# Performance work log

Measured on AMD Instinct MI355X. Metric: run time of the kernel, lower is better.

The kernel has to match this reference:

```python
import jax, jax.numpy as jnp
import numpy as np

V_DIM = 2048
Q_DIM = 1024
B = 64
K = 36


def setup_inputs() -> dict:
    key = jax.random.key(0)
    ks = jax.random.split(key, 6)
    s1 = 1.0 / np.sqrt(2 * V_DIM + Q_DIM)
    s2 = 1.0 / np.sqrt(V_DIM)
    s3 = 1.0 / np.sqrt(Q_DIM)
    return {
        "v": jax.random.normal(ks[0], (B, K, V_DIM), dtype=jnp.float32),
        "q": jax.random.normal(ks[1], (B, Q_DIM), dtype=jnp.float32),
        "W1": jax.random.normal(ks[2], (V_DIM, 2 * V_DIM + Q_DIM), dtype=jnp.float32) * s1,
        "b1": jnp.zeros((V_DIM,), dtype=jnp.float32),
        "W2": jax.random.normal(ks[3], (V_DIM, V_DIM), dtype=jnp.float32) * s2,
        "b2": jnp.zeros((V_DIM,), dtype=jnp.float32),
        "W3": jax.random.normal(ks[4], (Q_DIM, Q_DIM), dtype=jnp.float32) * s3,
        "b3": jnp.zeros((Q_DIM,), dtype=jnp.float32),
    }


def reference(v, q, W1, b1, W2, b2, W3, b3):
    # FCNet = (weight-normed) Linear + ReLU; dropout disabled (eval / p=0).
    vd = W2.shape[0]
    # q embedding: [B, q_dim]
    q_emb = jax.nn.relu(q @ W3.T + b3)
    # Decompose linear1(concat(v_i, v_j, q_emb)) into three matmuls.
    Wa = W1[:, :vd]            # acts on v_i
    Wb = W1[:, vd:2 * vd]      # acts on v_j
    Wc = W1[:, 2 * vd:]        # acts on q_emb
    a = jnp.einsum('bkd,vd->bkv', v, Wa)          # [B, K, v_dim]
    bpart = jnp.einsum('bkd,vd->bkv', v, Wb)      # [B, K, v_dim]
    c = jnp.einsum('bq,vq->bv', q_emb, Wc) + b1   # [B, v_dim]
    # Pairwise ReLU then sum over j: [B, K_i, K_j, v_dim] -> [B, K, v_dim]
    pair = jax.nn.relu(a[:, :, None, :] + bpart[:, None, :, :] + c[:, None, None, :])
    x = jnp.sum(pair, axis=2)
    # linear2 + ReLU
    return jax.nn.relu(jnp.einsum('bkv,wv->bkw', x, W2) + b2)
```

## Files before the change

kernel.cpp:

```cpp
#include <hip/hip_runtime.h>

#define V_DIMC 2048
#define Q_DIMC 1024
#define BATCH  64
#define KC     36
#define MROWS  (BATCH * KC)
#define W1LD   (2 * V_DIMC + Q_DIMC)

typedef __bf16 bf16_t;
typedef __attribute__((ext_vector_type(8))) __bf16 bf16x8;
typedef __attribute__((ext_vector_type(4))) __bf16 bf16x4;
typedef __attribute__((ext_vector_type(4))) float f32x4;

__device__ __forceinline__ void gload16(const bf16_t* g, bf16_t* l) {
    __builtin_amdgcn_global_load_lds(
        (const __attribute__((address_space(1))) unsigned int*)(g),
        (__attribute__((address_space(3))) unsigned int*)(l), 16, 0, 0);
}

#define MFMAI(a, b, c) __builtin_amdgcn_mfma_f32_16x16x32_bf16(a, b, c, 0, 0, 0)
#define BARX() __builtin_amdgcn_s_barrier()
#define LGKM0() asm volatile("s_waitcnt lgkmcnt(0)" ::: "memory")
#define VMC(n)  asm volatile("s_waitcnt vmcnt(" #n ")" ::: "memory")

__global__ __launch_bounds__(256) void conv_all(const float* __restrict__ v,
                                                const float* __restrict__ q,
                                                const float* __restrict__ W1,
                                                const float* __restrict__ W2,
                                                const float* __restrict__ W3,
                                                bf16_t* __restrict__ Wab,
                                                bf16_t* __restrict__ W2b,
                                                bf16_t* __restrict__ vb,
                                                bf16_t* __restrict__ W3b,
                                                bf16_t* __restrict__ Wcb,
                                                bf16_t* __restrict__ qb) {
    const int t = blockIdx.x * 256 + threadIdx.x;
    const float* src;
    bf16_t* dst;
    if (t < 2097152) {
        size_t idx = (size_t)t * 4;
        int row = (int)(idx >> 11), col = (int)(idx & 2047);
        src = (row < 2048) ? W1 + (size_t)row * W1LD + col
                           : W1 + (size_t)(row - 2048) * W1LD + V_DIMC + col;
        dst = Wab + idx;
    } else if (t < 3145728) {
        size_t idx = (size_t)(t - 2097152) * 4;
        src = W2 + idx; dst = W2b + idx;
    } else if (t < 4325376) {
        size_t idx = (size_t)(t - 3145728) * 4;
        src = v + idx; dst = vb + idx;
    } else if (t < 4587520) {
        size_t idx = (size_t)(t - 4325376) * 4;
        src = W3 + idx; dst = W3b + idx;
    } else if (t < 5111808) {
        size_t idx = (size_t)(t - 4587520) * 4;
        int row = (int)(idx >> 10), col = (int)(idx & 1023);
        src = W1 + (size_t)row * W1LD + 2 * V_DIMC + col;
        dst = Wcb + idx;
    } else {
        size_t idx = (size_t)(t - 5111808) * 4;
        src = q + idx; dst = qb + idx;
    }
    float4 f = *reinterpret_cast<const float4*>(src);
    bf16x4 o;
    o[0] = (bf16_t)f.x; o[1] = (bf16_t)f.y; o[2] = (bf16_t)f.z; o[3] = (bf16_t)f.w;
    *reinterpret_cast<bf16x4*>(dst) = o;
}

template <int MODE>
__global__ __launch_bounds__(512) void qgemm(const bf16_t* __restrict__ A,
                                             const bf16_t* __restrict__ B,
                                             void* __restrict__ out,
                                             const float* __restrict__ bias) {
    constexpr int K = 1024;
    constexpr int NDIM = (MODE == 0) ? Q_DIMC : V_DIMC;
    __shared__ float red[8][4096];
    const int tid = threadIdx.x;
    const int w = tid >> 6, l = tid & 63;
    const int n0 = blockIdx.x * 64;
    const int fr = l & 15, lq = l >> 4;
    const bf16_t* Ab = A + (size_t)(w * 128) + lq * 8;
    const bf16_t* Bb = B + (size_t)n0 * K + (size_t)(w * 128) + lq * 8;

    f32x4 acc[4][4] = {};
#pragma unroll
    for (int ks = 0; ks < 4; ++ks) {
        bf16x8 aF[4], bF[4];
#pragma unroll
        for (int mi = 0; mi < 4; ++mi)
            aF[mi] = *(const bf16x8*)(Ab + (size_t)(mi * 16 + fr) * K + ks * 32);
#pragma unroll
        for (int ni = 0; ni < 4; ++ni)
            bF[ni] = *(const bf16x8*)(Bb + (size_t)(ni * 16 + fr) * K + ks * 32);
#pragma unroll
        for (int mi = 0; mi < 4; ++mi)
#pragma unroll
            for (int ni = 0; ni < 4; ++ni)
                acc[mi][ni] = MFMAI(aF[mi], bF[ni], acc[mi][ni]);
    }

    const int rb = lq * 4;
#pragma unroll
    for (int mi = 0; mi < 4; ++mi)
#pragma unroll
        for (int ni = 0; ni < 4; ++ni)
#pragma unroll
            for (int j = 0; j < 4; ++j)
                red[w][(mi * 16 + rb + j) * 64 + ni * 16 + fr] = acc[mi][ni][j];
    __syncthreads();

    const int row = tid >> 3, cb = (tid & 7) * 8;
    float s[8] = {};
#pragma unroll
    for (int ww = 0; ww < 8; ++ww) {
        f32x4 v0 = *(const f32x4*)&red[ww][row * 64 + cb];
        f32x4 v1 = *(const f32x4*)&red[ww][row * 64 + cb + 4];
#pragma unroll
        for (int j = 0; j < 4; ++j) { s[j] += v0[j]; s[4 + j] += v1[j]; }
    }
    if (MODE == 0) {
        bf16x8 o;
#pragma unroll
        for (int j = 0; j < 8; ++j)
            o[j] = (bf16_t)fmaxf(s[j] + bias[n0 + cb + j], 0.f);
        *reinterpret_cast<bf16x8*>((bf16_t*)out + (size_t)row * NDIM + n0 + cb) = o;
    } else {
        float4 r0, r1;
        float* rr[2] = {&r0.x, &r1.x};
#pragma unroll
        for (int h = 0; h < 2; ++h)
#pragma unroll
            for (int j = 0; j < 4; ++j)
                rr[h][j] = s[h * 4 + j] + bias[n0 + cb + h * 4 + j];
        float* op = (float*)out + (size_t)row * NDIM + n0 + cb;
        *reinterpret_cast<float4*>(op) = r0;
        *reinterpret_cast<float4*>(op + 4) = r1;
    }
}

template <int MODE, int MF>
__global__ __launch_bounds__(512) void gemm8p(const bf16_t* __restrict__ A,
                                              const bf16_t* __restrict__ Bm,
                                              bf16_t* __restrict__ out0,
                                              bf16_t* __restrict__ out1,
                                              bf16_t* __restrict__ out2) {
    constexpr int K = 2048;
    constexpr int MH = MF / 2;
    const int z = (MODE == 2) ? (int)blockIdx.z : 0;
    const int NT = (MODE == 2) ? ((z == 2) ? 10 : 11) : 32;
    const int kb = (MODE == 2) ? z * 704 : 0;
    __shared__ bf16_t ldsA[2][MF * 2048];
    __shared__ bf16_t ldsB[2][2][8192];
    const int tid = threadIdx.x;
    const int w = tid >> 6, l = tid & 63;
    const int wm = w >> 2, wn = w & 3;
    const int m0 = blockIdx.y * (MF * 32);
    const int n0 = blockIdx.x * 256;
    const size_t sK = (size_t)K;

    const int arow = tid >> 3;
    const bf16_t* gA = A + (size_t)(m0 + arow) * sK + kb
                         + (size_t)(((tid & 7) ^ (arow & 7)) << 3);
    const int brow = tid >> 2;
    const bf16_t* gB = Bm + (size_t)(n0 + brow) * sK + kb
                          + (size_t)(((tid & 3) ^ ((tid >> 3) & 3)) << 3);
    const int stW = w * 512;

    auto STGA = [&](int T) {
#pragma unroll
        for (int p = 0; p < MH; ++p)
            gload16(gA + (size_t)(p * 64) * sK + (size_t)T * 64,
                    &ldsA[T & 1][p * 4096 + stW]);
    };
    auto STGB = [&](int ks, int T) {
        const bf16_t* g_ = gB + (size_t)T * 64 + ks * 32;
        gload16(g_, &ldsB[T & 1][ks][stW]);
        gload16(g_ + (size_t)128 * sK, &ldsB[T & 1][ks][4096 + stW]);
    };

    const int fr = l & 15, lq = l >> 4;
    const int sw0 = (lq ^ (fr & 7)) << 4;
    const int sw1 = ((4 | lq) ^ (fr & 7)) << 4;
    const int bsw = (lq ^ ((fr >> 1) & 3)) << 4;
    const int aro = fr * 128;
    const int bro = (wn * 64 + fr) * 64 + bsw;

    f32x4 acc[MF][4] = {};

    STGA(0);
    STGB(0, 0); STGB(1, 0);
    STGB(0, 1); STGB(1, 1);
    VMC(4);
    BARX();

    for (int T = 0; T < NT; ++T) {
        const char* pa  = (const char*)&ldsA[T & 1][0] + wm * (MF * 2048);
        const char* pb0 = (const char*)&ldsB[T & 1][0][0];
        const char* pb1 = (const char*)&ldsB[T & 1][1][0];
        bf16x8 aF[MH], bF[4];

#pragma unroll
        for (int mi = 0; mi < MH; ++mi)
            aF[mi] = *(const bf16x8*)(pa + mi * 2048 + aro + sw0);
#pragma unroll
        for (int ni = 0; ni < 4; ++ni)
            bF[ni] = *(const bf16x8*)(pb0 + bro + ni * 1024);
        if (T + 1 < NT) STGA(T + 1);
        BARX(); LGKM0();
        __builtin_amdgcn_s_setprio(1);
#pragma unroll
        for (int mi = 0; mi < MH; ++mi)
#pragma unroll
            for (int ni = 0; ni < 4; ++ni)
                acc[mi][ni] = MFMAI(aF[mi], bF[ni], acc[mi][ni]);
        __builtin_amdgcn_s_setprio(0);
        BARX();

#pragma unroll
        for (int mi = 0; mi < MH; ++mi)
            aF[mi] = *(const bf16x8*)(pa + MF * 1024 + mi * 2048 + aro + sw0);
        BARX(); LGKM0();
        __builtin_amdgcn_s_setprio(1);
#pragma unroll
        for (int mi = 0; mi < MH; ++mi)
#pragma unroll
            for (int ni = 0; ni < 4; ++ni)
                acc[MH + mi][ni] = MFMAI(aF[mi], bF[ni], acc[MH + mi][ni]);
        __builtin_amdgcn_s_setprio(0);
        BARX();

#pragma unroll
        for (int mi = 0; mi < MH; ++mi)
            aF[mi] = *(const bf16x8*)(pa + mi * 2048 + aro + sw1);
#pragma unroll
        for (int ni = 0; ni < 4; ++ni)
            bF[ni] = *(const bf16x8*)(pb1 + bro + ni * 1024);
        if (T + 2 < NT) STGB(0, T + 2);
        BARX(); LGKM0();
        __builtin_amdgcn_s_setprio(1);
#pragma unroll
        for (int mi = 0; mi < MH; ++mi)
#pragma unroll
            for (int ni = 0; ni < 4; ++ni)
                acc[mi][ni] = MFMAI(aF[mi], bF[ni], acc[mi][ni]);
        __builtin_amdgcn_s_setprio(0);
        BARX();

#pragma unroll
        for (int mi = 0; mi < MH; ++mi)
            aF[mi] = *(const bf16x8*)(pa + MF * 1024 + mi * 2048 + aro + sw1);
        if (T + 2 < NT) STGB(1, T + 2);
        BARX(); LGKM0();
        __builtin_amdgcn_s_setprio(1);
#pragma unroll
        for (int mi = 0; mi < MH; ++mi)
#pragma unroll
            for (int ni = 0; ni < 4; ++ni)
                acc[MH + mi][ni] = MFMAI(aF[mi], bF[ni], acc[MH + mi][ni]);
        __builtin_amdgcn_s_setprio(0);
        if (T < NT - 2) { VMC(4); } else { VMC(0); }
        BARX();
    }

    bf16_t* o;
    int gn0;
    if (MODE == 0) {
        if (n0 < V_DIMC) { o = out0; gn0 = n0; }
        else             { o = out1; gn0 = n0 - V_DIMC; }
    } else {
        o = (z == 0) ? out0 : (z == 1) ? out1 : out2;
        gn0 = n0;
    }
    const int rb = lq * 4;
#pragma unroll
    for (int mi = 0; mi < MF; ++mi)
#pragma unroll
        for (int ni = 0; ni < 4; ++ni) {
            const size_t gm = (size_t)(m0 + wm * (MF * 16) + mi * 16 + rb);
            const int gn = gn0 + wn * 64 + ni * 16 + fr;
#pragma unroll
            for (int r = 0; r < 4; ++r)
                o[(gm + r) * V_DIMC + gn] = (bf16_t)acc[mi][ni][r];
        }
}

__global__ __launch_bounds__(256) void reduce_out(const bf16_t* __restrict__ p0,
                                                  const bf16_t* __restrict__ p1,
                                                  const bf16_t* __restrict__ p2,
                                                  const float* __restrict__ b2,
                                                  float* __restrict__ out) {
    const size_t t = (size_t)blockIdx.x * 256 + threadIdx.x;
    const size_t idx = t * 8;
    bf16x8 a = *reinterpret_cast<const bf16x8*>(p0 + idx);
    bf16x8 b = *reinterpret_cast<const bf16x8*>(p1 + idx);
    bf16x8 c = *reinterpret_cast<const bf16x8*>(p2 + idx);
    const int col = (int)(idx & (V_DIMC - 1));
    float4 r0, r1;
    float* rr[2] = {&r0.x, &r1.x};
#pragma unroll
    for (int h = 0; h < 2; ++h)
#pragma unroll
        for (int j = 0; j < 4; ++j)
            rr[h][j] = fmaxf((float)a[h * 4 + j] + (float)b[h * 4 + j] +
                             (float)c[h * 4 + j] + b2[col + h * 4 + j], 0.f);
    *reinterpret_cast<float4*>(out + idx) = r0;
    *reinterpret_cast<float4*>(out + idx + 4) = r1;
}

__global__ __launch_bounds__(256) void pair_kernel(const bf16_t* __restrict__ A,
                                                   const bf16_t* __restrict__ Bp,
                                                   const float* __restrict__ cbuf,
                                                   bf16_t* __restrict__ X) {
    const int v = blockIdx.x * 256 + threadIdx.x;
    const int b = blockIdx.y;
    const float cc = cbuf[b * V_DIMC + v];
    const bf16_t* Ab = A + (size_t)b * KC * V_DIMC + v;
    const bf16_t* Bb = Bp + (size_t)b * KC * V_DIMC + v;
    float av[KC], bv[KC];
#pragma unroll
    for (int k = 0; k < KC; ++k) {
        av[k] = (float)Ab[(size_t)k * V_DIMC] + cc;
        bv[k] = (float)Bb[(size_t)k * V_DIMC];
    }
    bf16_t* Xb = X + (size_t)b * KC * V_DIMC + v;
#pragma unroll
    for (int k = 0; k < KC; ++k) {
        float s = 0.f;
#pragma unroll
        for (int j = 0; j < KC; ++j) s += fmaxf(av[k] + bv[j], 0.f);
        Xb[(size_t)k * V_DIMC] = (bf16_t)s;
    }
}

extern "C" void kernel_launch(void* const* d_in, const int* in_sizes, int n_in,
                              void* d_out, int out_size, void* d_ws, size_t ws_size,
                              hipStream_t stream) {
    const float* v  = (const float*)d_in[0];
    const float* q  = (const float*)d_in[1];
    const float* W1 = (const float*)d_in[2];
    const float* b1 = (const float*)d_in[3];
    const float* W2 = (const float*)d_in[4];
    const float* b2 = (const float*)d_in[5];
    const float* W3 = (const float*)d_in[6];
    const float* b3 = (const float*)d_in[7];
    float* out = (float*)d_out;

    char* wsb = (char*)d_ws;
    bf16_t* Wab_b = (bf16_t*)wsb;
    bf16_t* W2b   = (bf16_t*)(wsb + 16777216ull);
    bf16_t* vb    = (bf16_t*)(wsb + 25165824ull);
    bf16_t* Abf   = (bf16_t*)(wsb + 34603008ull);
    bf16_t* W3b   = (bf16_t*)(wsb + 34603008ull);
    bf16_t* Wcb   = (bf16_t*)(wsb + 34603008ull + 2097152);
    bf16_t* qb    = (bf16_t*)(wsb + 34603008ull + 6291456);
    bf16_t* Bbf   = (bf16_t*)(wsb + 44040192ull);
    bf16_t* qemb  = (bf16_t*)(wsb + 53477376ull);
    float*  cbuf  = (float*) (wsb + 53608448ull);
    bf16_t* Xb    = Wab_b;

    conv_all<<<dim3(20032), 256, 0, stream>>>(v, q, W1, W2, W3, Wab_b, W2b, vb, W3b, Wcb, qb);
    qgemm<0><<<dim3(Q_DIMC / 64), 512, 0, stream>>>(qb, W3b, qemb, b3);
    qgemm<1><<<dim3(V_DIMC / 64), 512, 0, stream>>>(qemb, Wcb, cbuf, b1);

    gemm8p<0, 6><<<dim3(4096 / 256, MROWS / 192), 512, 0, stream>>>(vb, Wab_b, Abf, Bbf, nullptr);
    pair_kernel<<<dim3(V_DIMC / 256, BATCH), 256, 0, stream>>>(Abf, Bbf, cbuf, Xb);
    gemm8p<2, 8><<<dim3(V_DIMC / 256, MROWS / 256, 3), 512, 0, stream>>>(Xb, W2b, Abf, Bbf, vb);
    reduce_out<<<dim3((MROWS * V_DIMC / 8) / 256), 256, 0, stream>>>(Abf, Bbf, vb, b2, out);
}
```

Measured before the change: 147.1 us.

## Restructure GEMM pipeline to two phases per tile and remap blocks across XCDs

Cuts the inner K-loop from four barrier-separated MFMA phases to two by loading all MF A fragments at once. B staging is now one tile ahead instead of two, with explicit vmcnt waits placed inside each phase. For MODE 0 it also remaps the flat block index so that blocks sharing the same A and B tiles land on the same XCD, aiming for better L2 reuse. The trade-offs are higher register pressure from the larger aF array and less prefetch distance for B.

New measurement: 139.8 us, median of 3. 1.05x faster.

```diff
diff --git a/kernel.cpp b/kernel.cpp
--- a/kernel.cpp
+++ b/kernel.cpp
@@ -154,8 +154,18 @@
     const int tid = threadIdx.x;
     const int w = tid >> 6, l = tid & 63;
     const int wm = w >> 2, wn = w & 3;
-    const int m0 = blockIdx.y * (MF * 32);
-    const int n0 = blockIdx.x * 256;
+
+    int bx, by;
+    if (MODE == 0) {
+        const int flat = (int)blockIdx.y * 16 + (int)blockIdx.x;
+        const int xcd = flat & 7, idx = flat >> 3;
+        bx = (xcd & 3) * 4 + (idx & 3);
+        by = (xcd >> 2) * 6 + (idx >> 2);
+    } else {
+        bx = (int)blockIdx.x; by = (int)blockIdx.y;
+    }
+    const int m0 = by * (MF * 32);
+    const int n0 = bx * 256;
     const size_t sK = (size_t)K;
 
     const int arow = tid >> 3;
@@ -188,28 +198,33 @@
     f32x4 acc[MF][4] = {};
 
     STGA(0);
-    STGB(0, 0); STGB(1, 0);
-    STGB(0, 1); STGB(1, 1);
-    VMC(4);
+    STGB(0, 0);
+    STGB(1, 0);
+    VMC(2);
     BARX();
 
     for (int T = 0; T < NT; ++T) {
         const char* pa  = (const char*)&ldsA[T & 1][0] + wm * (MF * 2048);
         const char* pb0 = (const char*)&ldsB[T & 1][0][0];
         const char* pb1 = (const char*)&ldsB[T & 1][1][0];
-        bf16x8 aF[MH], bF[4];
-
-#pragma unroll
-        for (int mi = 0; mi < MH; ++mi)
+        bf16x8 aF[MF], bF[4];
+
+#pragma unroll
+        for (int mi = 0; mi < MF; ++mi)
             aF[mi] = *(const bf16x8*)(pa + mi * 2048 + aro + sw0);
 #pragma unroll
         for (int ni = 0; ni < 4; ++ni)
             bF[ni] = *(const bf16x8*)(pb0 + bro + ni * 1024);
-        if (T + 1 < NT) STGA(T + 1);
+        if (T + 1 < NT) {
+            STGA(T + 1); STGB(0, T + 1);
+            if constexpr (MF == 6) { VMC(5); } else { VMC(6); }
+        } else {
+            VMC(0);
+        }
         BARX(); LGKM0();
         __builtin_amdgcn_s_setprio(1);
 #pragma unroll
-        for (int mi = 0; mi < MH; ++mi)
+        for (int mi = 0; mi < MF; ++mi)
 #pragma unroll
             for (int ni = 0; ni < 4; ++ni)
                 acc[mi][ni] = MFMAI(aF[mi], bF[ni], acc[mi][ni]);
@@ -217,48 +232,25 @@
         BARX();
 
 #pragma unroll
-        for (int mi = 0; mi < MH; ++mi)
-            aF[mi] = *(const bf16x8*)(pa + MF * 1024 + mi * 2048 + aro + sw0);
+        for (int mi = 0; mi < MF; ++mi)
+            aF[mi] = *(const bf16x8*)(pa + mi * 2048 + aro + sw1);
+#pragma unroll
+        for (int ni = 0; ni < 4; ++ni)
+            bF[ni] = *(const bf16x8*)(pb1 + bro + ni * 1024);
+        if (T + 1 < NT) {
+            STGB(1, T + 1);
+            VMC(2);
+        } else {
+            VMC(0);
+        }
         BARX(); LGKM0();
         __builtin_amdgcn_s_setprio(1);
 #pragma unroll
-        for (int mi = 0; mi < MH; ++mi)
-#pragma unroll
-            for (int ni = 0; ni < 4; ++ni)
-                acc[MH + mi][ni] = MFMAI(aF[mi], bF[ni], acc[MH + mi][ni]);
-        __builtin_amdgcn_s_setprio(0);
-        BARX();
-
-#pragma unroll
-        for (int mi = 0; mi < MH; ++mi)
-            aF[mi] = *(const bf16x8*)(pa + mi * 2048 + aro + sw1);
-#pragma unroll
-        for (int ni = 0; ni < 4; ++ni)
-            bF[ni] = *(const bf16x8*)(pb1 + bro + ni * 1024);
-        if (T + 2 < NT) STGB(0, T + 2);
-        BARX(); LGKM0();
-        __builtin_amdgcn_s_setprio(1);
-#pragma unroll
-        for (int mi = 0; mi < MH; ++mi)
+        for (int mi = 0; mi < MF; ++mi)
 #pragma unroll
             for (int ni = 0; ni < 4; ++ni)
                 acc[mi][ni] = MFMAI(aF[mi], bF[ni], acc[mi][ni]);
         __builtin_amdgcn_s_setprio(0);
-        BARX();
-
-#pragma unroll
-        for (int mi = 0; mi < MH; ++mi)
-            aF[mi] = *(const bf16x8*)(pa + MF * 1024 + mi * 2048 + aro + sw1);
-        if (T + 2 < NT) STGB(1, T + 2);
-        BARX(); LGKM0();
-        __builtin_amdgcn_s_setprio(1);
-#pragma unroll
-        for (int mi = 0; mi < MH; ++mi)
-#pragma unroll
-            for (int ni = 0; ni < 4; ++ni)
-                acc[MH + mi][ni] = MFMAI(aF[mi], bF[ni], acc[MH + mi][ni]);
-        __builtin_amdgcn_s_setprio(0);
-        if (T < NT - 2) { VMC(4); } else { VMC(0); }
         BARX();
     }
 
```
